# Kernel optimization log

Hardware: AMD Instinct MI355X
Metric: run time of the kernel (lower is better)

## Reference

```python
import jax, jax.numpy as jnp
import numpy as np

M = 255   # filter_order
P = 80    # frame_period


def setup_inputs() -> dict:
    key = jax.random.key(0)
    k1, k2 = jax.random.split(key)
    B, N = 8, 800
    T = N * P
    x = jax.random.normal(k1, (B, T), dtype=jnp.float32)
    h = jax.random.normal(k2, (B, N, M + 1), dtype=jnp.float32)
    return {"x": x, "h": h}


def _zerodf(x, h):
    # x: (B, T) excitation; h: (B, N, M+1) per-frame FIR coefficients, T = N*P
    B, T = x.shape
    N = h.shape[1]
    # left-pad with M zeros, then sliding windows of length M+1, stride 1
    x_pad = jnp.pad(x, ((0, 0), (M, 0)))                       # (B, T+M)
    idx = jnp.arange(T)[:, None] + jnp.arange(M + 1)[None, :]  # (T, M+1)
    xw = x_pad[:, idx]                                         # (B, T, M+1); window t = [x[t-M], ..., x[t]]
    # flip coeffs so xw . h_flip = sum_m h_m[t] * x[t-m]
    hf = h[..., ::-1]                                          # (B, N, M+1)
    # linear interpolation of coeffs from frame rate to sample rate,
    # holding the last frame (replicate pad): w[n*P+k] = lerp(h[n], h[n+1], k/P)
    hp = jnp.concatenate([hf, hf[:, -1:, :]], axis=1)          # (B, N+1, M+1)
    frac = (jnp.arange(P, dtype=x.dtype) / P)[None, None, :, None]  # (1,1,P,1)
    hi = hp[:, :-1, None, :] * (1.0 - frac) + hp[:, 1:, None, :] * frac  # (B,N,P,M+1)
    hi = hi.reshape(B, N * P, M + 1)                           # (B, T, M+1)
    return jnp.sum(xw * hi, axis=-1)                           # (B, T)


def reference(x, h):
    return _zerodf(x, h)
```

## Files before the change

kernel.cpp:

```cpp
#include <hip/hip_runtime.h>


#define TAPS 256
#define PP 80
#define BB 8
#define NN 800
#define TT (NN * PP)
#define FPB 8
#define TPF 16
#define RR 5
#define NTHREADS (FPB * TPF)
#define HSTRIDE 260
#define XWIN (FPB * PP + TAPS - 1)
#define CHUNKS (NN / FPB)

__global__ __launch_bounds__(NTHREADS) void azdf_kernel(
    const float* __restrict__ x, const float* __restrict__ h,
    float* __restrict__ out)
{
    __shared__ float sh[(FPB + 1) * HSTRIDE];
    __shared__ float sx[XWIN + 1];

    const int tid = threadIdx.x;
    const int blk = blockIdx.x;
    const int b   = blk / CHUNKS;
    const int nc  = blk % CHUNKS;
    const int n0  = nc * FPB;
    const int t0  = n0 * PP;

    const float* hb = h + (size_t)b * NN * TAPS;
    for (int i4 = tid; i4 < (FPB + 1) * (TAPS / 4); i4 += NTHREADS) {
        int r  = i4 >> 6;
        int k4 = i4 & 63;
        int gr = n0 + r;
        if (gr > NN - 1) gr = NN - 1;
        float4 v = ((const float4*)(hb + (size_t)gr * TAPS))[k4];
        ((float4*)(sh + r * HSTRIDE))[k4] = v;
    }

    const float* xb = x + (size_t)b * TT;
    for (int i = tid; i < XWIN; i += NTHREADS) {
        int g = t0 - (TAPS - 1) + i;
        sx[i] = (g >= 0) ? xb[g] : 0.0f;
    }
    __syncthreads();

    const int lf   = tid / TPF;
    const int lane = tid % TPF;
    const int p0   = lane * RR;
    const float* h0 = sh + lf * HSTRIDE;
    const float* h1 = h0 + HSTRIDE;
    const int base = lf * PP + p0 + (TAPS - 1);

    float acc0[RR], acc1[RR];
    #pragma unroll
    for (int r = 0; r < RR; ++r) { acc0[r] = 0.0f; acc1[r] = 0.0f; }

    for (int k = 0; k < TAPS; k += 4) {
        float xv[RR + 3];
        #pragma unroll
        for (int j = 0; j < RR + 3; ++j) xv[j] = sx[base - k - 3 + j];
        #pragma unroll
        for (int d = 0; d < 4; ++d) {
            float c0 = h0[k + d];
            float c1 = h1[k + d];
            #pragma unroll
            for (int r = 0; r < RR; ++r) {
                float xr = xv[r + 3 - d];
                acc0[r] = fmaf(xr, c0, acc0[r]);
                acc1[r] = fmaf(xr, c1, acc1[r]);
            }
        }
    }

    float* ob = out + (size_t)b * TT + t0 + lf * PP + p0;
    #pragma unroll
    for (int r = 0; r < RR; ++r) {
        float f = (float)(p0 + r) * (1.0f / PP);
        ob[r] = acc0[r] + f * (acc1[r] - acc0[r]);
    }
}

extern "C" void kernel_launch(void* const* d_in, const int* in_sizes, int n_in,
                              void* d_out, int out_size, void* d_ws, size_t ws_size,
                              hipStream_t stream) {
    const float* x = (const float*)d_in[0];
    const float* h = (const float*)d_in[1];
    float* out    = (float*)d_out;
    azdf_kernel<<<BB * CHUNKS, NTHREADS, 0, stream>>>(x, h, out);
}
```

Baseline: 71.39 us.

## Split tap reduction across two thread halves and halve frames per block

Each block now covers 4 frames instead of 8, and its 128 threads split the 256 taps into two halves, combining partial sums through shared memory before the lerp and store. The tap loop is fully unrolled with 8-wide steps and a rolling x register window, and launch bounds ask for 4 blocks per CU. The goal is more blocks and waves for better occupancy and latency hiding on this small grid. The cost is an extra barrier, a shared-memory reduction, and more redundant h and x loading per output, since block overlap grows.

After: 70.90 us. Within noise of the previous version (-0.7%).

```diff
diff --git a/kernel.cpp b/kernel.cpp
--- a/kernel.cpp
+++ b/kernel.cpp
@@ -6,20 +6,23 @@
 #define BB 8
 #define NN 800
 #define TT (NN * PP)
-#define FPB 8
+#define FPB 4
 #define TPF 16
 #define RR 5
-#define NTHREADS (FPB * TPF)
+#define KSPLIT 2
+#define KTH (TAPS / KSPLIT)
+#define NTHREADS (KSPLIT * FPB * TPF)
 #define HSTRIDE 260
 #define XWIN (FPB * PP + TAPS - 1)
 #define CHUNKS (NN / FPB)
 
-__global__ __launch_bounds__(NTHREADS) void azdf_kernel(
+__global__ __launch_bounds__(NTHREADS, 4) void azdf_kernel(
     const float* __restrict__ x, const float* __restrict__ h,
     float* __restrict__ out)
 {
     __shared__ float sh[(FPB + 1) * HSTRIDE];
     __shared__ float sx[XWIN + 1];
+    __shared__ float red[FPB * TPF * 2 * RR];
 
     const int tid = threadIdx.x;
     const int blk = blockIdx.x;
@@ -34,8 +37,8 @@
         int k4 = i4 & 63;
         int gr = n0 + r;
         if (gr > NN - 1) gr = NN - 1;
-        float4 v = ((const float4*)(hb + (size_t)gr * TAPS))[k4];
-        ((float4*)(sh + r * HSTRIDE))[k4] = v;
+        ((float4*)(sh + r * HSTRIDE))[k4] =
+            ((const float4*)(hb + (size_t)gr * TAPS))[k4];
     }
 
     const float* xb = x + (size_t)b * TT;
@@ -45,39 +48,59 @@
     }
     __syncthreads();
 
-    const int lf   = tid / TPF;
-    const int lane = tid % TPF;
+    const int kh   = tid >> 6;
+    const int lf   = (tid >> 4) & (FPB - 1);
+    const int lane = tid & 15;
     const int p0   = lane * RR;
-    const float* h0 = sh + lf * HSTRIDE;
+    const float* h0 = sh + lf * HSTRIDE + kh * KTH;
     const float* h1 = h0 + HSTRIDE;
-    const int base = lf * PP + p0 + (TAPS - 1);
+    const int base = lf * PP + p0 + (TAPS - 1) - kh * KTH;
 
     float acc0[RR], acc1[RR];
     #pragma unroll
     for (int r = 0; r < RR; ++r) { acc0[r] = 0.0f; acc1[r] = 0.0f; }
 
-    for (int k = 0; k < TAPS; k += 4) {
-        float xv[RR + 3];
+    float xv[12];
+    #pragma unroll
+    for (int j = 8; j < 12; ++j) xv[j] = sx[base - 7 + j];
+
+    #pragma unroll
+    for (int i = 0; i < KTH / 8; ++i) {
+        const int k = i * 8;
+        if (i > 0) {
+            xv[8] = xv[0]; xv[9] = xv[1]; xv[10] = xv[2]; xv[11] = xv[3];
+        }
         #pragma unroll
-        for (int j = 0; j < RR + 3; ++j) xv[j] = sx[base - k - 3 + j];
+        for (int j = 0; j < 8; ++j) xv[j] = sx[base - k - 7 + j];
+
         #pragma unroll
-        for (int d = 0; d < 4; ++d) {
+        for (int d = 0; d < 8; ++d) {
             float c0 = h0[k + d];
             float c1 = h1[k + d];
             #pragma unroll
             for (int r = 0; r < RR; ++r) {
-                float xr = xv[r + 3 - d];
+                float xr = xv[r + 7 - d];
                 acc0[r] = fmaf(xr, c0, acc0[r]);
                 acc1[r] = fmaf(xr, c1, acc1[r]);
             }
         }
     }
 
-    float* ob = out + (size_t)b * TT + t0 + lf * PP + p0;
-    #pragma unroll
-    for (int r = 0; r < RR; ++r) {
-        float f = (float)(p0 + r) * (1.0f / PP);
-        ob[r] = acc0[r] + f * (acc1[r] - acc0[r]);
+    float* pr = red + (lf * TPF + lane) * (2 * RR);
+    if (kh == 1) {
+        #pragma unroll
+        for (int r = 0; r < RR; ++r) { pr[r] = acc0[r]; pr[RR + r] = acc1[r]; }
+    }
+    __syncthreads();
+    if (kh == 0) {
+        float* ob = out + (size_t)b * TT + t0 + lf * PP + p0;
+        #pragma unroll
+        for (int r = 0; r < RR; ++r) {
+            float a0 = acc0[r] + pr[r];
+            float a1 = acc1[r] + pr[RR + r];
+            float f  = (float)(p0 + r) * (1.0f / PP);
+            ob[r] = a0 + f * (a1 - a0);
+        }
     }
 }
 
```
